# Kernel tuning notes

Hardware: AMD Instinct MI355X
Metric: run time of the kernel (lower is better)

The kernel has to match this reference:

```python
import jax, jax.numpy as jnp
import numpy as np

L, B, C, OUT = 4, 4, 256, 4
H, W = 128, 128
HEADS, DH, G = 8, 32, 64
N = H * W
INNER = HEADS * DH
HID = 4 * C


def _ln(x, w, b, eps=1e-5):
    m = jnp.mean(x, -1, keepdims=True)
    v = jnp.mean((x - m) ** 2, -1, keepdims=True)
    return (x - m) / jnp.sqrt(v + eps) * w + b


def setup_inputs() -> dict:
    key = jax.random.key(0)
    ks = iter(jax.random.split(key, 16))
    nrm = lambda shape, s=0.02: jax.random.normal(next(ks), shape, jnp.float32) * s
    return dict(
        fx=jax.random.normal(next(ks), (B, N, C), jnp.float32),
        ln1_w=jnp.ones((L, C)), ln1_b=jnp.zeros((L, C)),
        convx_w=nrm((L, 3, 3, C, INNER)), convx_b=jnp.zeros((L, INNER)),
        convfx_w=nrm((L, 3, 3, C, INNER)), convfx_b=jnp.zeros((L, INNER)),
        slice_w=nrm((L, DH, G)), slice_b=jnp.zeros((L, G)),
        temperature=0.5 * jnp.ones((L, HEADS)),
        wq=nrm((L, DH, DH)), wk=nrm((L, DH, DH)), wv=nrm((L, DH, DH)),
        wo=nrm((L, INNER, C)), bo=jnp.zeros((L, C)),
        ln2_w=jnp.ones((L, C)), ln2_b=jnp.zeros((L, C)),
        w1=nrm((L, C, HID)), b1=jnp.zeros((L, HID)),
        w2=nrm((L, HID, C)), b2=jnp.zeros((L, C)),
        ln3_w=jnp.ones((C,)), ln3_b=jnp.zeros((C,)),
        w_out=nrm((C, OUT)), b_out=jnp.zeros((OUT,)),
    )


def reference(fx, ln1_w, ln1_b, convx_w, convx_b, convfx_w, convfx_b,
              slice_w, slice_b, temperature, wq, wk, wv, wo, bo,
              ln2_w, ln2_b, w1, b1, w2, b2, ln3_w, ln3_b, w_out, b_out):
    Bb = fx.shape[0]
    scale = DH ** -0.5
    for i in range(L):
        # --- Physics attention (slice attention) ---
        x = _ln(fx, ln1_w[i], ln1_b[i])
        ximg = x.reshape(Bb, H, W, C)  # NHWC
        conv = lambda w, b: jax.lax.conv_general_dilated(
            ximg, w, (1, 1), 'SAME',
            dimension_numbers=('NHWC', 'HWIO', 'NHWC')) + b
        fx_mid = conv(convfx_w[i], convfx_b[i]).reshape(Bb, N, HEADS, DH).transpose(0, 2, 1, 3)  # [B,h,N,d]
        x_mid = conv(convx_w[i], convx_b[i]).reshape(Bb, N, HEADS, DH).transpose(0, 2, 1, 3)
        temp = jnp.clip(temperature[i], 0.1, 5.0)[None, :, None, None]
        logits = (jnp.einsum('bhnd,dg->bhng', x_mid, slice_w[i]) + slice_b[i]) / temp
        sw = jax.nn.softmax(logits, axis=-1)  # [B,h,N,G]
        norm = sw.sum(2)  # [B,h,G]
        st = jnp.einsum('bhnc,bhng->bhgc', fx_mid, sw) / (norm + 1e-5)[..., None]  # [B,h,G,d]
        q = jnp.einsum('bhgc,cd->bhgd', st, wq[i])
        k = jnp.einsum('bhgc,cd->bhgd', st, wk[i])
        v = jnp.einsum('bhgc,cd->bhgd', st, wv[i])
        attn = jax.nn.softmax(jnp.einsum('bhgd,bhkd->bhgk', q, k) * scale, axis=-1)
        ot = jnp.einsum('bhgk,bhkd->bhgd', attn, v)  # [B,h,G,d]
        out_x = jnp.einsum('bhgc,bhng->bhnc', ot, sw)  # deslice back to points
        out_x = out_x.transpose(0, 2, 1, 3).reshape(Bb, N, INNER)
        fx = fx + out_x @ wo[i] + bo[i]
        # --- MLP (n_layers=0, no res inside) ---
        h = _ln(fx, ln2_w[i], ln2_b[i])
        h = jax.nn.gelu(h @ w1[i] + b1[i], approximate=False) @ w2[i] + b2[i]
        fx = fx + h
    # last-layer head
    return _ln(fx, ln3_w, ln3_b) @ w_out + b_out
```

## Files before the change

kernel.cpp:

```cpp
#include <hip/hip_runtime.h>
#include <hip/hip_bf16.h>

typedef __hip_bfloat16 bf16;
typedef __bf16 bfv8 __attribute__((ext_vector_type(8)));
typedef float f32x4 __attribute__((ext_vector_type(4)));

#define BB 4
#define HH 128
#define WWI 128
#define NN 16384
#define CC 256
#define LL 4
#define NHEADS 8
#define DHD 32
#define GG 64
#define INNERC 256
#define HIDD 1024
#define SPLIT 32
#define SSP 16

__device__ __forceinline__ float b2f(bf16 x) { return __bfloat162float(x); }
__device__ __forceinline__ bf16 f2b(float x) { return __float2bfloat16(x); }
__device__ __forceinline__ float us2f(unsigned short v) {
  return __uint_as_float(((unsigned)v) << 16);
}
__device__ __forceinline__ unsigned short b2us(bf16 h) {
  union { bf16 b; unsigned short u; } c; c.b = h; return c.u;
}

__device__ __forceinline__ void async16(void* l, const void* g) {
  __builtin_amdgcn_global_load_lds(
      (const __attribute__((address_space(1))) void*)g,
      (__attribute__((address_space(3))) void*)l, 16, 0, 0);
}

__device__ __forceinline__ float wave_sum(float v) {
#pragma unroll
  for (int off = 32; off > 0; off >>= 1) v += __shfl_down(v, off, 64);
  return v;
}

__device__ __forceinline__ float gelu_exact(float x) {
  return 0.5f * x * (1.0f + erff(x * 0.70710678118654752f));
}

__global__ void transpose_cast_kernel(const float* __restrict__ src, bf16* __restrict__ dst,
                                      int R, int Cm) {
  __shared__ float tile[32][33];
  int tb = blockIdx.z;
  const float* s = src + (size_t)tb * R * Cm;
  bf16* d = dst + (size_t)tb * R * Cm;
  int c0 = blockIdx.x * 32, r0 = blockIdx.y * 32;
  int tx = threadIdx.x & 31, ty = threadIdx.x >> 5;
  for (int rr = ty; rr < 32; rr += 8) {
    int r = r0 + rr, c = c0 + tx;
    tile[rr][tx] = (r < R && c < Cm) ? s[(size_t)r * Cm + c] : 0.f;
  }
  __syncthreads();
  for (int cc = ty; cc < 32; cc += 8) {
    int c = c0 + cc, r = r0 + tx;
    if (c < Cm && r < R) d[(size_t)c * R + r] = f2b(tile[tx][cc]);
  }
}

__global__ __launch_bounds__(256) void ln_kernel(const float* __restrict__ x,
                                                 const float* __restrict__ w,
                                                 const float* __restrict__ b,
                                                 bf16* __restrict__ out) {
  int wid = threadIdx.x >> 6, lane = threadIdx.x & 63;
  int p = blockIdx.x * 4 + wid;
  float4 v = ((const float4*)(x + (size_t)p * CC))[lane];
  float s = v.x + v.y + v.z + v.w;
  float sq = v.x * v.x + v.y * v.y + v.z * v.z + v.w * v.w;
#pragma unroll
  for (int off = 32; off > 0; off >>= 1) {
    s += __shfl_xor(s, off, 64);
    sq += __shfl_xor(sq, off, 64);
  }
  float mean = s * (1.0f / CC);
  float var = sq * (1.0f / CC) - mean * mean;
  float rstd = rsqrtf(var + 1e-5f);
  float4 wv = ((const float4*)w)[lane];
  float4 bv = ((const float4*)b)[lane];
  unsigned short o0 = b2us(f2b((v.x - mean) * rstd * wv.x + bv.x));
  unsigned short o1 = b2us(f2b((v.y - mean) * rstd * wv.y + bv.y));
  unsigned short o2 = b2us(f2b((v.z - mean) * rstd * wv.z + bv.z));
  unsigned short o3 = b2us(f2b((v.w - mean) * rstd * wv.w + bv.w));
  uint2 pk = make_uint2((unsigned)o0 | ((unsigned)o1 << 16),
                        (unsigned)o2 | ((unsigned)o3 << 16));
  ((uint2*)(out + (size_t)p * CC))[lane] = pk;
}

__global__ __launch_bounds__(512, 2) void conv_mfma_kernel(
    const bf16* __restrict__ xln, const bf16* __restrict__ wt,
    const float* __restrict__ bias, bf16* __restrict__ out,
    const float* __restrict__ zbuf) {
  __shared__ __align__(16) unsigned short As[4 * 130 * 64];
  __shared__ __align__(16) unsigned short Bsm[2][256 * 64];
  int bid = blockIdx.x;
  bid = (bid & 7) * 32 + (bid >> 3);
  int h0 = (bid & 63) * 2;
  int b = bid >> 6;
  int t = threadIdx.x, lane = t & 63, wid = t >> 6;
  int r = wid & 1;
  int wn = (wid >> 1) * 64;
  int l15 = lane & 15, l4 = lane >> 4;
  int wu = t & ~63;
  f32x4 acc[8][4];
#pragma unroll
  for (int mi = 0; mi < 8; ++mi)
#pragma unroll
    for (int ni = 0; ni < 4; ++ni) acc[mi][ni] = (f32x4){0.f, 0.f, 0.f, 0.f};
  const bf16* xbase = xln + (size_t)b * NN * CC;

  auto stageB = [&](int buf, int tap, int q) {
#pragma unroll
    for (int k = 0; k < 4; ++k) {
      int u = t + k * 512;
      int n = u >> 3, jp = u & 7, j = jp ^ (n & 7);
      async16(&Bsm[buf][(size_t)(wu + k * 512) * 8],
              wt + ((size_t)(tap * 256 + n)) * 256 + q * 64 + j * 8);
    }
  };

  for (int q = 0; q < 4; ++q) {
#pragma unroll
    for (int k = 0; k < 8; ++k) {
      int u = t + k * 512;
      int jp = u & 7, pc = u >> 3;
      int ar = pc / 130, cl = pc - ar * 130;
      int j = jp ^ (cl & 7);
      int gr = h0 + ar - 1, gc = cl - 1;
      const void* src =
          ((unsigned)gr < 128u && (unsigned)gc < 128u)
              ? (const void*)(xbase + ((size_t)(gr * WWI + gc)) * CC + q * 64 + j * 8)
              : (const void*)zbuf;
      async16(&As[(size_t)(wu + k * 512) * 8], src);
    }
    if (t < 64) {
      int u = t + 4096;
      int jp = u & 7, pc = u >> 3;
      int ar = pc / 130, cl = pc - ar * 130;
      int j = jp ^ (cl & 7);
      int gr = h0 + ar - 1, gc = cl - 1;
      const void* src =
          ((unsigned)gr < 128u && (unsigned)gc < 128u)
              ? (const void*)(xbase + ((size_t)(gr * WWI + gc)) * CC + q * 64 + j * 8)
              : (const void*)zbuf;
      async16(&As[(size_t)4096 * 8], src);
    }
    if (q == 0) stageB(0, 0, 0);
    __syncthreads();

    for (int tap = 0; tap < 9; ++tap) {
      int cur = (q * 9 + tap) & 1;
      if (tap < 8)      stageB(cur ^ 1, tap + 1, q);
      else if (q < 3)   stageB(cur ^ 1, 0, q + 1);
      int ky = tap / 3, kx = tap - ky * 3;
      const unsigned short* Bc = Bsm[cur];
#pragma unroll
      for (int s = 0; s < 2; ++s) {
        bfv8 af[8], bfr[4];
#pragma unroll
        for (int mi = 0; mi < 8; ++mi) {
          int cl = mi * 16 + l15 + kx;
          af[mi] = *(const bfv8*)(&As[((size_t)((ky + r) * 130 + cl)) * 64 +
                                      (((s * 4 + l4) ^ (cl & 7)) << 3)]);
        }
#pragma unroll
        for (int ni = 0; ni < 4; ++ni) {
          int rn = wn + ni * 16 + l15;
          bfr[ni] = *(const bfv8*)(&Bc[(size_t)rn * 64 + (((s * 4 + l4) ^ (rn & 7)) << 3)]);
        }
#pragma unroll
        for (int mi = 0; mi < 8; ++mi)
#pragma unroll
          for (int ni = 0; ni < 4; ++ni)
            acc[mi][ni] = __builtin_amdgcn_mfma_f32_16x16x32_bf16(af[mi], bfr[ni], acc[mi][ni], 0, 0, 0);
      }
      __syncthreads();
    }
  }
  int colB = wn + l15;
  int rowB = l4 * 4;
#pragma unroll
  for (int ni = 0; ni < 4; ++ni) {
    int oc = colB + ni * 16;
    float bv = bias[oc];
#pragma unroll
    for (int mi = 0; mi < 8; ++mi) {
#pragma unroll
      for (int rr = 0; rr < 4; ++rr) {
        int pix = mi * 16 + rowB + rr;
        out[((size_t)(b * NN + (h0 + r) * WWI + pix)) * CC + oc] = f2b(acc[mi][ni][rr] + bv);
      }
    }
  }
}

__global__ __launch_bounds__(512) void gemm_ln_kernel(
    const bf16* __restrict__ A, const bf16* __restrict__ BT,
    const float* __restrict__ bias, float* __restrict__ fx,
    const float* __restrict__ lw, const float* __restrict__ lb,
    bf16* __restrict__ xout) {
  __shared__ __align__(16) unsigned short As[128 * 64];
  __shared__ __align__(16) unsigned short Bs[256 * 64];
  int z = blockIdx.y;
  const bf16* Aa = A + (size_t)z * NN * 512;
  const bf16* Ba = BT + (size_t)z * 256 * 512;
  size_t fb = (size_t)z * NN * 256;
  int m0 = blockIdx.x * 128;
  int t = threadIdx.x, lane = t & 63, wid = t >> 6;
  int wm = (wid & 1) * 64, wn = (wid >> 1) * 64;
  int l15 = lane & 15, q4 = lane >> 4;
  int wu = t & ~63;
  f32x4 acc[4][4];
#pragma unroll
  for (int mi = 0; mi < 4; ++mi)
#pragma unroll
    for (int ni = 0; ni < 4; ++ni) acc[mi][ni] = (f32x4){0.f, 0.f, 0.f, 0.f};

  for (int kb = 0; kb < 512; kb += 64) {
    __syncthreads();
#pragma unroll
    for (int i = 0; i < 2; ++i) {
      int u = t + i * 512;
      int row = u >> 3, jp = u & 7, j = jp ^ (row & 7);
      async16(&As[(size_t)(wu + i * 512) * 8], Aa + (size_t)(m0 + row) * 512 + kb + j * 8);
    }
#pragma unroll
    for (int i = 0; i < 4; ++i) {
      int u = t + i * 512;
      int n = u >> 3, jp = u & 7, j = jp ^ (n & 7);
      async16(&Bs[(size_t)(wu + i * 512) * 8], Ba + (size_t)n * 512 + kb + j * 8);
    }
    __syncthreads();
#pragma unroll
    for (int s = 0; s < 2; ++s) {
      int kgrp = s * 4 + q4;
      bfv8 af[4], bfr[4];
#pragma unroll
      for (int mi = 0; mi < 4; ++mi) {
        int row = wm + mi * 16 + l15;
        af[mi] = *(const bfv8*)(&As[(size_t)row * 64 + ((kgrp ^ (row & 7)) << 3)]);
      }
#pragma unroll
      for (int ni = 0; ni < 4; ++ni) {
        int n = wn + ni * 16 + l15;
        bfr[ni] = *(const bfv8*)(&Bs[(size_t)n * 64 + ((kgrp ^ (n & 7)) << 3)]);
      }
#pragma unroll
      for (int mi = 0; mi < 4; ++mi)
#pragma unroll
        for (int ni = 0; ni < 4; ++ni)
          acc[mi][ni] = __builtin_amdgcn_mfma_f32_16x16x32_bf16(af[mi], bfr[ni], acc[mi][ni], 0, 0, 0);
    }
  }
  __syncthreads();
  float* rs = (float*)As;
  float* rq = rs + 512;
  int cw = wid >> 1;
  int colB = wn + l15;
  float bv[4], lwv[4], lbv[4];
#pragma unroll
  for (int ni = 0; ni < 4; ++ni) {
    bv[ni] = bias[colB + ni * 16];
    lwv[ni] = lw[colB + ni * 16];
    lbv[ni] = lb[colB + ni * 16];
  }
#pragma unroll
  for (int mi = 0; mi < 4; ++mi) {
#pragma unroll
    for (int r = 0; r < 4; ++r) {
      int row = m0 + wm + mi * 16 + q4 * 4 + r;
      float s = 0.f, sq = 0.f;
#pragma unroll
      for (int ni = 0; ni < 4; ++ni) {
        size_t idx = fb + (size_t)row * 256 + colB + ni * 16;
        float v = fx[idx] + acc[mi][ni][r] + bv[ni];
        fx[idx] = v;
        s += v; sq += v * v;
      }
#pragma unroll
      for (int off = 1; off < 16; off <<= 1) {
        s += __shfl_xor(s, off, 64);
        sq += __shfl_xor(sq, off, 64);
      }
      if (l15 == 0) {
        int lrow = wm + mi * 16 + q4 * 4 + r;
        rs[cw * 128 + lrow] = s;
        rq[cw * 128 + lrow] = sq;
      }
    }
  }
  __syncthreads();
#pragma unroll
  for (int mi = 0; mi < 4; ++mi) {
#pragma unroll
    for (int r = 0; r < 4; ++r) {
      int lrow = wm + mi * 16 + q4 * 4 + r;
      float tot = rs[lrow] + rs[128 + lrow] + rs[256 + lrow] + rs[384 + lrow];
      float totq = rq[lrow] + rq[128 + lrow] + rq[256 + lrow] + rq[384 + lrow];
      float mean = tot * (1.0f / CC);
      float var = totq * (1.0f / CC) - mean * mean;
      float rstd = rsqrtf(var + 1e-5f);
      int row = m0 + lrow;
#pragma unroll
      for (int ni = 0; ni < 4; ++ni) {
        size_t idx = fb + (size_t)row * 256 + colB + ni * 16;
        float v = fx[idx];
        xout[idx] = f2b((v - mean) * rstd * lwv[ni] + lbv[ni]);
      }
    }
  }
}

__global__ __launch_bounds__(512, 4) void mlp_fused_kernel(
    const bf16* __restrict__ xln, const bf16* __restrict__ w1t,
    const float* __restrict__ b1, const bf16* __restrict__ w2t,
    const float* __restrict__ b2, float* __restrict__ fx,
    const float* __restrict__ lnw, const float* __restrict__ lnb,
    bf16* __restrict__ xout) {
  __shared__ __align__(16) unsigned short As[64 * 256];
  __shared__ __align__(16) bf16 Hs[64 * 128];
  __shared__ __align__(16) unsigned short Wb[256 * 64];
  int m0 = blockIdx.x * 64;
  int t = threadIdx.x, lane = t & 63, wid = t >> 6;
  int l15 = lane & 15, q4 = lane >> 4;
  int wm2 = (wid & 1) * 32, wn2 = (wid >> 1) * 32;
  int wm = (wid & 1) * 32, wn = (wid >> 1) * 64;

  const unsigned short* xg = (const unsigned short*)xln + (size_t)m0 * 256;
#pragma unroll
  for (int i = 0; i < 4; ++i) {
    int u = t + i * 512;
    int row = u >> 5, v = u & 31;
    int kb = v >> 3, jp = v & 7;
    uint4 val = ((const uint4*)xg)[u];
    ((uint4*)As)[row * 32 + kb * 8 + (jp ^ (row & 7))] = val;
  }

  f32x4 accO[2][4];
#pragma unroll
  for (int mi = 0; mi < 2; ++mi)
#pragma unroll
    for (int ni = 0; ni < 4; ++ni) accO[mi][ni] = (f32x4){0.f, 0.f, 0.f, 0.f};

  for (int j = 0; j < 8; ++j) {
    int hbase = j * 128;
    f32x4 acc2[2][2];
#pragma unroll
    for (int mi = 0; mi < 2; ++mi)
#pragma unroll
      for (int nj = 0; nj < 2; ++nj) acc2[mi][nj] = (f32x4){0.f, 0.f, 0.f, 0.f};
    for (int kb = 0; kb < 4; ++kb) {
      __syncthreads();
#pragma unroll
      for (int i = 0; i < 2; ++i) {
        int u = t + i * 512;
        int n = u >> 3, jp = u & 7;
        uint4 val = *(const uint4*)(w1t + (size_t)(hbase + n) * 256 + kb * 64 + jp * 8);
        ((uint4*)Wb)[n * 8 + (jp ^ (n & 7))] = val;
      }
      __syncthreads();
#pragma unroll
      for (int ks = 0; ks < 2; ++ks) {
        int kgrp = ks * 4 + q4;
        bfv8 af[2], bfr[2];
#pragma unroll
        for (int mi = 0; mi < 2; ++mi) {
          int row = wm2 + mi * 16 + l15;
          af[mi] = *(const bfv8*)(&As[row * 256 + kb * 64 + ((kgrp ^ (row & 7)) << 3)]);
        }
#pragma unroll
        for (int nj = 0; nj < 2; ++nj) {
          int n = wn2 + nj * 16 + l15;
          bfr[nj] = *(const bfv8*)(&Wb[n * 64 + ((kgrp ^ (n & 7)) << 3)]);
        }
#pragma unroll
        for (int mi = 0; mi < 2; ++mi)
#pragma unroll
          for (int nj = 0; nj < 2; ++nj)
            acc2[mi][nj] = __builtin_amdgcn_mfma_f32_16x16x32_bf16(af[mi], bfr[nj], acc2[mi][nj], 0, 0, 0);
      }
    }
#pragma unroll
    for (int nj = 0; nj < 2; ++nj) {
      int coln = wn2 + nj * 16 + l15;
      float bv = b1[hbase + coln];
      int half = coln >> 6, sub = (coln >> 3) & 7, lo = coln & 7;
#pragma unroll
      for (int mi = 0; mi < 2; ++mi) {
#pragma unroll
        for (int r = 0; r < 4; ++r) {
          int row = wm2 + mi * 16 + q4 * 4 + r;
          float v = acc2[mi][nj][r] + bv;
          Hs[row * 128 + half * 64 + (((sub ^ (row & 7)) << 3) + lo)] = f2b(gelu_exact(v));
        }
      }
    }
    for (int kb2 = 0; kb2 < 2; ++kb2) {
      __syncthreads();
#pragma unroll
      for (int i = 0; i < 4; ++i) {
        int u = t + i * 512;
        int n = u >> 3, jp = u & 7;
        uint4 val = *(const uint4*)(w2t + (size_t)n * 1024 + hbase + kb2 * 64 + jp * 8);
        ((uint4*)Wb)[n * 8 + (jp ^ (n & 7))] = val;
      }
      __syncthreads();
#pragma unroll
      for (int ks = 0; ks < 2; ++ks) {
        int kgrp = ks * 4 + q4;
        bfv8 af[2], bfr[4];
#pragma unroll
        for (int mi = 0; mi < 2; ++mi) {
          int row = wm + mi * 16 + l15;
          af[mi] = *(const bfv8*)(&Hs[row * 128 + kb2 * 64 + ((kgrp ^ (row & 7)) << 3)]);
        }
#pragma unroll
        for (int ni = 0; ni < 4; ++ni) {
          int n = wn + ni * 16 + l15;
          bfr[ni] = *(const bfv8*)(&Wb[n * 64 + ((kgrp ^ (n & 7)) << 3)]);
        }
#pragma unroll
        for (int mi = 0; mi < 2; ++mi)
#pragma unroll
          for (int ni = 0; ni < 4; ++ni)
            accO[mi][ni] = __builtin_amdgcn_mfma_f32_16x16x32_bf16(af[mi], bfr[ni], accO[mi][ni], 0, 0, 0);
      }
    }
  }
  float* rs = (float*)As;
  float* rq = rs + 256;
  int cw = wid >> 1;
  int colB = wn + l15;
  float bv[4], lwv[4], lbv[4];
#pragma unroll
  for (int ni = 0; ni < 4; ++ni) {
    bv[ni] = b2[colB + ni * 16];
    if (lnw) { lwv[ni] = lnw[colB + ni * 16]; lbv[ni] = lnb[colB + ni * 16]; }
  }
#pragma unroll
  for (int mi = 0; mi < 2; ++mi) {
#pragma unroll
    for (int r = 0; r < 4; ++r) {
      int row = m0 + wm + mi * 16 + q4 * 4 + r;
      float s = 0.f, sq = 0.f;
#pragma unroll
      for (int ni = 0; ni < 4; ++ni) {
        size_t idx = (size_t)row * 256 + colB + ni * 16;
        float v = fx[idx] + accO[mi][ni][r] + bv[ni];
        fx[idx] = v;
        s += v; sq += v * v;
      }
      if (lnw) {
#pragma unroll
        for (int off = 1; off < 16; off <<= 1) {
          s += __shfl_xor(s, off, 64);
          sq += __shfl_xor(sq, off, 64);
        }
        if (l15 == 0) {
          int lrow = wm + mi * 16 + q4 * 4 + r;
          rs[cw * 64 + lrow] = s;
          rq[cw * 64 + lrow] = sq;
        }
      }
    }
  }
  if (lnw) {
    __syncthreads();
#pragma unroll
    for (int mi = 0; mi < 2; ++mi) {
#pragma unroll
      for (int r = 0; r < 4; ++r) {
        int lrow = wm + mi * 16 + q4 * 4 + r;
        float tot = rs[lrow] + rs[64 + lrow] + rs[128 + lrow] + rs[192 + lrow];
        float totq = rq[lrow] + rq[64 + lrow] + rq[128 + lrow] + rq[192 + lrow];
        float mean = tot * (1.0f / CC);
        float var = totq * (1.0f / CC) - mean * mean;
        float rstd = rsqrtf(var + 1e-5f);
        int row = m0 + lrow;
#pragma unroll
        for (int ni = 0; ni < 4; ++ni) {
          size_t idx = (size_t)row * 256 + colB + ni * 16;
          float v = fx[idx];
          xout[idx] = f2b((v - mean) * rstd * lwv[ni] + lbv[ni]);
        }
      }
    }
  }
}

__global__ __launch_bounds__(256) void slice_softmax_kernel(
    const bf16* __restrict__ xmid, const float* __restrict__ sw_w,
    const float* __restrict__ sw_b, const float* __restrict__ temp,
    bf16* __restrict__ swout) {
  __shared__ float xm[SSP][256];
  int p0 = blockIdx.x * SSP;
  int t = threadIdx.x;
  int g = t & 63, pq = t >> 6;
  float wreg[32];
#pragma unroll
  for (int d = 0; d < 32; ++d) wreg[d] = sw_w[d * 64 + g];
  float bg = sw_b[g];
  float rt[8];
#pragma unroll
  for (int h = 0; h < 8; ++h) rt[h] = 1.0f / fminf(fmaxf(temp[h], 0.1f), 5.0f);
  const unsigned short* xg = (const unsigned short*)xmid + (size_t)p0 * 256;
#pragma unroll
  for (int i2 = t; i2 < SSP * 32; i2 += 256) {
    uint4 v = ((const uint4*)xg)[i2];
    int p = i2 >> 5, c = (i2 & 31) << 3;
    xm[p][c + 0] = us2f((unsigned short)(v.x & 0xffff));
    xm[p][c + 1] = us2f((unsigned short)(v.x >> 16));
    xm[p][c + 2] = us2f((unsigned short)(v.y & 0xffff));
    xm[p][c + 3] = us2f((unsigned short)(v.y >> 16));
    xm[p][c + 4] = us2f((unsigned short)(v.z & 0xffff));
    xm[p][c + 5] = us2f((unsigned short)(v.z >> 16));
    xm[p][c + 6] = us2f((unsigned short)(v.w & 0xffff));
    xm[p][c + 7] = us2f((unsigned short)(v.w >> 16));
  }
  __syncthreads();
  for (int pp2 = 0; pp2 < SSP / 4; ++pp2) {
    int p = pp2 * 4 + pq;
#pragma unroll
    for (int h = 0; h < NHEADS; ++h) {
      float acc = bg;
      const float* xr = &xm[p][h * 32];
#pragma unroll
      for (int d = 0; d < 32; ++d) acc += xr[d] * wreg[d];
      float logit = acc * rt[h];
      float m = logit;
#pragma unroll
      for (int off = 32; off > 0; off >>= 1) m = fmaxf(m, __shfl_xor(m, off, 64));
      float e = __expf(logit - m);
      float s = e;
#pragma unroll
      for (int off = 32; off > 0; off >>= 1) s += __shfl_xor(s, off, 64);
      swout[(size_t)(p0 + p) * 512 + h * 64 + g] = f2b(e / s);
    }
  }
}

__global__ __launch_bounds__(256) void slice_st_kernel(
    const bf16* __restrict__ fxmid, const bf16* __restrict__ sw,
    float* __restrict__ stp, float* __restrict__ normp) {
  __shared__ __align__(16) unsigned short sw_s[64 * 64];
  __shared__ __align__(16) unsigned short fx_s[32 * 64];
  __shared__ float npart[2][64];
  int split = blockIdx.x, h = blockIdx.y, b = blockIdx.z;
  int t = threadIdx.x, w = t >> 6, lane = t & 63;
  int l15 = lane & 15, q4 = lane >> 4;
  int ns0 = split * (NN / SPLIT);
  const int NT = (NN / SPLIT) / 64;
  f32x4 acc0 = {0.f, 0.f, 0.f, 0.f}, acc1 = {0.f, 0.f, 0.f, 0.f};
  float nacc = 0.f;
  const unsigned short* swg = (const unsigned short*)sw + (size_t)b * NN * 512 + h * 64;
  const unsigned short* fxg = (const unsigned short*)fxmid + (size_t)b * NN * 256 + h * 32;

  for (int kt = 0; kt < NT; ++kt) {
    int n0 = ns0 + kt * 64;
    __syncthreads();
    if (w < 2) {
      int g = lane;
#pragma unroll
      for (int i = 0; i < 4; ++i) {
        int j = w + 2 * i;
        const unsigned short* p = swg + (size_t)(n0 + j * 8) * 512 + g;
        unsigned short v0 = p[0],     v1 = p[512],  v2 = p[1024], v3 = p[1536];
        unsigned short v4 = p[2048],  v5 = p[2560], v6 = p[3072], v7 = p[3584];
        nacc += us2f(v0) + us2f(v1) + us2f(v2) + us2f(v3) +
                us2f(v4) + us2f(v5) + us2f(v6) + us2f(v7);
        uint4 pk = make_uint4((unsigned)v0 | ((unsigned)v1 << 16),
                              (unsigned)v2 | ((unsigned)v3 << 16),
                              (unsigned)v4 | ((unsigned)v5 << 16),
                              (unsigned)v6 | ((unsigned)v7 << 16));
        ((uint4*)sw_s)[g * 8 + (j ^ (g & 7))] = pk;
      }
    } else {
      int d = lane & 31, nh = lane >> 5, w3 = w - 2;
#pragma unroll
      for (int i = 0; i < 2; ++i) {
        int nbase = (w3 * 2 + i) * 16 + nh * 8;
        const unsigned short* p = fxg + (size_t)(n0 + nbase) * 256 + d;
        unsigned short v0 = p[0],    v1 = p[256],  v2 = p[512],  v3 = p[768];
        unsigned short v4 = p[1024], v5 = p[1280], v6 = p[1536], v7 = p[1792];
        uint4 pk = make_uint4((unsigned)v0 | ((unsigned)v1 << 16),
                              (unsigned)v2 | ((unsigned)v3 << 16),
                              (unsigned)v4 | ((unsigned)v5 << 16),
                              (unsigned)v6 | ((unsigned)v7 << 16));
        int u = nbase >> 3;
        ((uint4*)fx_s)[d * 8 + (u ^ (d & 7))] = pk;
      }
    }
    __syncthreads();
    int gg = w * 16 + l15;
    int d0 = l15, d1 = 16 + l15;
#pragma unroll
    for (int ks = 0; ks < 2; ++ks) {
      bfv8 af  = ((const bfv8*)sw_s)[gg * 8 + ((ks * 4 + q4) ^ (gg & 7))];
      bfv8 bf0 = ((const bfv8*)fx_s)[d0 * 8 + ((ks * 4 + q4) ^ (d0 & 7))];
      bfv8 bf1 = ((const bfv8*)fx_s)[d1 * 8 + ((ks * 4 + q4) ^ (d1 & 7))];
      acc0 = __builtin_amdgcn_mfma_f32_16x16x32_bf16(af, bf0, acc0, 0, 0, 0);
      acc1 = __builtin_amdgcn_mfma_f32_16x16x32_bf16(af, bf1, acc1, 0, 0, 0);
    }
  }
  if (w < 2) npart[w][lane] = nacc;
  __syncthreads();
  int bh = b * NHEADS + h;
  if (t < 64) normp[(size_t)split * (BB * NHEADS * GG) + bh * 64 + t] = npart[0][t] + npart[1][t];
  size_t base = ((size_t)split * (BB * NHEADS * GG) + bh * 64) * 32;
#pragma unroll
  for (int r = 0; r < 4; ++r) {
    int g = w * 16 + q4 * 4 + r;
    stp[base + (size_t)g * 32 + l15] = acc0[r];
    stp[base + (size_t)g * 32 + 16 + l15] = acc1[r];
  }
}

__global__ __launch_bounds__(256) void attn_wc_kernel(
    const float* __restrict__ stp, const float* __restrict__ normp,
    const float* __restrict__ wq, const float* __restrict__ wk,
    const float* __restrict__ wv, const float* __restrict__ wo,
    bf16* __restrict__ wct) {
  __shared__ float wqs[32 * 32], wks[32 * 32], wvs[32 * 32];
  __shared__ float st[GG][DHD + 1];
  __shared__ float qq[GG][DHD + 1], kk[GG][DHD + 1], vv[GG][DHD + 1];
  __shared__ float pm[GG][GG + 1];
  __shared__ float nrm[GG];
  int bh = blockIdx.x;
  int h2 = bh & 7, bq = bh >> 3;
  int t = threadIdx.x;
  ((float4*)wqs)[t] = ((const float4*)wq)[t];
  ((float4*)wks)[t] = ((const float4*)wk)[t];
  ((float4*)wvs)[t] = ((const float4*)wv)[t];
  float wol[DHD];
#pragma unroll
  for (int d = 0; d < DHD; ++d) wol[d] = wo[(size_t)(h2 * DHD + d) * CC + t];
  if (t < 64) {
    float ns = 0.f;
    for (int s = 0; s < SPLIT; ++s) ns += normp[(size_t)s * (BB * NHEADS * GG) + bh * 64 + t];
    nrm[t] = 1.0f / (ns + 1e-5f);
  }
  __syncthreads();
#pragma unroll
  for (int i = 0; i < 8; ++i) {
    int idx = t + i * 256;
    int g = idx >> 5, d = idx & 31;
    float a = 0.f;
    for (int s = 0; s < SPLIT; ++s)
      a += stp[((size_t)s * (BB * NHEADS * GG) + bh * 64 + g) * 32 + d];
    st[g][d] = a * nrm[g];
  }
  __syncthreads();
#pragma unroll
  for (int i = 0; i < 8; ++i) {
    int idx = t + i * 256;
    int g = idx >> 5, d = idx & 31;
    float aq = 0.f, ak = 0.f, av = 0.f;
#pragma unroll
    for (int c = 0; c < 32; ++c) {
      float sv = st[g][c];
      aq += sv * wqs[c * 32 + d];
      ak += sv * wks[c * 32 + d];
      av += sv * wvs[c * 32 + d];
    }
    qq[g][d] = aq; kk[g][d] = ak; vv[g][d] = av;
  }
  __syncthreads();
  {
    int g = t >> 2, sub = t & 3;
    float sc[16];
    float m = -1e30f;
    const float scale = 0.17677669529663687f;
#pragma unroll
    for (int jj = 0; jj < 16; ++jj) {
      int j = sub * 16 + jj;
      float a = 0.f;
#pragma unroll
      for (int d = 0; d < 32; ++d) a += qq[g][d] * kk[j][d];
      a *= scale;
      sc[jj] = a;
      m = fmaxf(m, a);
    }
    m = fmaxf(m, __shfl_xor(m, 1, 64));
    m = fmaxf(m, __shfl_xor(m, 2, 64));
    float ssum = 0.f;
#pragma unroll
    for (int jj = 0; jj < 16; ++jj) { sc[jj] = __expf(sc[jj] - m); ssum += sc[jj]; }
    ssum += __shfl_xor(ssum, 1, 64);
    ssum += __shfl_xor(ssum, 2, 64);
    float rs = 1.0f / ssum;
#pragma unroll
    for (int jj = 0; jj < 16; ++jj) pm[g][sub * 16 + jj] = sc[jj] * rs;
  }
  __syncthreads();
#pragma unroll
  for (int i = 0; i < 8; ++i) {
    int idx = t + i * 256;
    int g = idx >> 5, d = idx & 31;
    float a = 0.f;
#pragma unroll
    for (int j = 0; j < GG; ++j) a += pm[g][j] * vv[j][d];
    qq[g][d] = a;
  }
  __syncthreads();
  bf16* dst = wct + ((size_t)bq * CC + t) * (NHEADS * GG) + h2 * GG;
#pragma unroll 4
  for (int g = 0; g < GG; ++g) {
    float a = 0.f;
#pragma unroll
    for (int d = 0; d < DHD; ++d) a += wol[d] * qq[g][d];
    dst[g] = f2b(a);
  }
}

__global__ __launch_bounds__(256) void head_kernel(const float* __restrict__ fx,
                                                   const float* __restrict__ w,
                                                   const float* __restrict__ b,
                                                   const float* __restrict__ wout,
                                                   const float* __restrict__ bout,
                                                   float* __restrict__ out) {
  int wid = threadIdx.x >> 6, lane = threadIdx.x & 63;
  int p = blockIdx.x * 4 + wid;
  float4 v = ((const float4*)(fx + (size_t)p * CC))[lane];
  float s = v.x + v.y + v.z + v.w;
  float sq = v.x * v.x + v.y * v.y + v.z * v.z + v.w * v.w;
#pragma unroll
  for (int off = 32; off > 0; off >>= 1) {
    s += __shfl_xor(s, off, 64);
    sq += __shfl_xor(sq, off, 64);
  }
  float mean = s * (1.0f / CC);
  float var = sq * (1.0f / CC) - mean * mean;
  float rstd = rsqrtf(var + 1e-5f);
  float4 wv = ((const float4*)w)[lane];
  float4 bv = ((const float4*)b)[lane];
  float xn0 = (v.x - mean) * rstd * wv.x + bv.x;
  float xn1 = (v.y - mean) * rstd * wv.y + bv.y;
  float xn2 = (v.z - mean) * rstd * wv.z + bv.z;
  float xn3 = (v.w - mean) * rstd * wv.w + bv.w;
  float4 w0 = ((const float4*)wout)[lane * 4 + 0];
  float4 w1 = ((const float4*)wout)[lane * 4 + 1];
  float4 w2 = ((const float4*)wout)[lane * 4 + 2];
  float4 w3 = ((const float4*)wout)[lane * 4 + 3];
  float4 o;
  o.x = xn0 * w0.x + xn1 * w1.x + xn2 * w2.x + xn3 * w3.x;
  o.y = xn0 * w0.y + xn1 * w1.y + xn2 * w2.y + xn3 * w3.y;
  o.z = xn0 * w0.z + xn1 * w1.z + xn2 * w2.z + xn3 * w3.z;
  o.w = xn0 * w0.w + xn1 * w1.w + xn2 * w2.w + xn3 * w3.w;
#pragma unroll
  for (int off = 32; off > 0; off >>= 1) {
    o.x += __shfl_xor(o.x, off, 64);
    o.y += __shfl_xor(o.y, off, 64);
    o.z += __shfl_xor(o.z, off, 64);
    o.w += __shfl_xor(o.w, off, 64);
  }
  if (lane == 0) {
    float4 bo4 = *((const float4*)bout);
    float4 r;
    r.x = o.x + bo4.x; r.y = o.y + bo4.y; r.z = o.z + bo4.z; r.w = o.w + bo4.w;
    ((float4*)out)[p] = r;
  }
}

extern "C" void kernel_launch(void* const* d_in, const int* in_sizes, int n_in,
                              void* d_out, int out_size, void* d_ws, size_t ws_size,
                              hipStream_t stream) {
  const float* fx_in      = (const float*)d_in[0];
  const float* ln1_w      = (const float*)d_in[1];
  const float* ln1_b      = (const float*)d_in[2];
  const float* convx_w    = (const float*)d_in[3];
  const float* convx_b    = (const float*)d_in[4];
  const float* convfx_w   = (const float*)d_in[5];
  const float* convfx_b   = (const float*)d_in[6];
  const float* slice_w    = (const float*)d_in[7];
  const float* slice_b    = (const float*)d_in[8];
  const float* temperature= (const float*)d_in[9];
  const float* wq         = (const float*)d_in[10];
  const float* wk         = (const float*)d_in[11];
  const float* wv         = (const float*)d_in[12];
  const float* wo         = (const float*)d_in[13];
  const float* bo         = (const float*)d_in[14];
  const float* ln2_w      = (const float*)d_in[15];
  const float* ln2_b      = (const float*)d_in[16];
  const float* w1         = (const float*)d_in[17];
  const float* b1         = (const float*)d_in[18];
  const float* w2         = (const float*)d_in[19];
  const float* b2         = (const float*)d_in[20];
  const float* ln3_w      = (const float*)d_in[21];
  const float* ln3_b      = (const float*)d_in[22];
  const float* w_out      = (const float*)d_in[23];
  const float* b_out      = (const float*)d_in[24];
  float* out = (float*)d_out;

  char* ws = (char*)d_ws;
  size_t off = 0;
  auto alloc = [&](size_t bytes) -> void* {
    void* p = ws + off;
    off += (bytes + 255) & ~(size_t)255;
    return p;
  };
  float* fx32  = (float*)alloc((size_t)BB * NN * CC * 4);
  bf16* xln    = (bf16*)alloc((size_t)BB * NN * CC * 2);
  char* uni    = (char*)alloc((size_t)BB * NN * 512 * 2 * 2);
  bf16* xmid   = (bf16*)uni;
  bf16* fxmid  = (bf16*)(uni + (size_t)BB * NN * INNERC * 2);
  bf16* swb    = (bf16*)(uni + (size_t)2 * BB * NN * INNERC * 2);
  float* stp   = (float*)uni;
  float* normp = (float*)(uni + (size_t)SPLIT * BB * NHEADS * GG * DHD * 4);
  bf16* wtx    = (bf16*)alloc((size_t)LL * 9 * CC * INNERC * 2);
  bf16* wtfx   = (bf16*)alloc((size_t)LL * 9 * CC * INNERC * 2);
  bf16* w1t    = (bf16*)alloc((size_t)LL * CC * HIDD * 2);
  bf16* w2t    = (bf16*)alloc((size_t)LL * HIDD * CC * 2);
  bf16* wct    = (bf16*)alloc((size_t)BB * CC * NHEADS * GG * 2);
  float* zbuf  = (float*)alloc(256);
  (void)ws_size; (void)in_sizes; (void)n_in; (void)out_size;

  hipMemsetAsync(zbuf, 0, 256, stream);

  transpose_cast_kernel<<<dim3(8, 8, LL * 9), 256, 0, stream>>>(convx_w, wtx, CC, INNERC);
  transpose_cast_kernel<<<dim3(8, 8, LL * 9), 256, 0, stream>>>(convfx_w, wtfx, CC, INNERC);
  transpose_cast_kernel<<<dim3(32, 8, LL), 256, 0, stream>>>(w1, w1t, CC, HIDD);
  transpose_cast_kernel<<<dim3(8, 32, LL), 256, 0, stream>>>(w2, w2t, HIDD, CC);

  hipMemcpyAsync(fx32, fx_in, (size_t)BB * NN * CC * sizeof(float),
                 hipMemcpyDeviceToDevice, stream);

  const int M = BB * NN;
  ln_kernel<<<M / 4, 256, 0, stream>>>(fx32, ln1_w, ln1_b, xln);
  for (int i = 0; i < LL; ++i) {
    conv_mfma_kernel<<<BB * HH / 2, 512, 0, stream>>>(
        xln, wtfx + (size_t)i * 9 * CC * INNERC, convfx_b + i * INNERC, fxmid,
        (const float*)zbuf);
    conv_mfma_kernel<<<BB * HH / 2, 512, 0, stream>>>(
        xln, wtx + (size_t)i * 9 * CC * INNERC, convx_b + i * INNERC, xmid,
        (const float*)zbuf);
    slice_softmax_kernel<<<M / SSP, 256, 0, stream>>>(
        xmid, slice_w + i * DHD * GG, slice_b + i * GG, temperature + i * NHEADS, swb);
    slice_st_kernel<<<dim3(SPLIT, NHEADS, BB), 256, 0, stream>>>(fxmid, swb, stp, normp);
    attn_wc_kernel<<<BB * NHEADS, 256, 0, stream>>>(
        stp, normp, wq + i * DHD * DHD, wk + i * DHD * DHD, wv + i * DHD * DHD,
        wo + (size_t)i * INNERC * CC, wct);
    gemm_ln_kernel<<<dim3(NN / 128, BB), 512, 0, stream>>>(
        swb, wct, bo + i * CC, fx32, ln2_w + i * CC, ln2_b + i * CC, xln);
    const float* nlw = (i < LL - 1) ? ln1_w + (i + 1) * CC : nullptr;
    const float* nlb = (i < LL - 1) ? ln1_b + (i + 1) * CC : nullptr;
    mlp_fused_kernel<<<M / 64, 512, 0, stream>>>(
        xln, w1t + (size_t)i * CC * HIDD, b1 + i * HIDD,
        w2t + (size_t)i * HIDD * CC, b2 + i * CC, fx32, nlw, nlb, xln);
  }
  head_kernel<<<M / 4, 256, 0, stream>>>(fx32, ln3_w, ln3_b, w_out, b_out, out);
}
```

Measured before the change: 2.394 ms.

## Unfuse next-layer LayerNorm from MLP kernel; keep residual values in registers for LN

The MLP kernel no longer computes the following layer's LayerNorm in its epilogue. It only adds the residual, and a separate ln_kernel launch produces the normalized bf16 input for layers after the first. In gemm_ln_kernel the updated residual values are kept in a register array instead of being re-read from global memory for normalization. This lightens the MLP epilogue (fewer registers, no extra syncthreads) at the cost of an extra kernel launch and an extra full pass over fx. The register array also raises register pressure in gemm_ln.

```diff
diff --git a/kernel.cpp b/kernel.cpp
--- a/kernel.cpp
+++ b/kernel.cpp
@@ -268,6 +268,7 @@
     lwv[ni] = lw[colB + ni * 16];
     lbv[ni] = lb[colB + ni * 16];
   }
+  float vkeep[4][4][4];
 #pragma unroll
   for (int mi = 0; mi < 4; ++mi) {
 #pragma unroll
@@ -279,6 +280,7 @@
         size_t idx = fb + (size_t)row * 256 + colB + ni * 16;
         float v = fx[idx] + acc[mi][ni][r] + bv[ni];
         fx[idx] = v;
+        vkeep[mi][r][ni] = v;
         s += v; sq += v * v;
       }
 #pragma unroll
@@ -308,7 +310,7 @@
 #pragma unroll
       for (int ni = 0; ni < 4; ++ni) {
         size_t idx = fb + (size_t)row * 256 + colB + ni * 16;
-        float v = fx[idx];
+        float v = vkeep[mi][r][ni];
         xout[idx] = f2b((v - mean) * rstd * lwv[ni] + lbv[ni]);
       }
     }
@@ -318,9 +320,7 @@
 __global__ __launch_bounds__(512, 4) void mlp_fused_kernel(
     const bf16* __restrict__ xln, const bf16* __restrict__ w1t,
     const float* __restrict__ b1, const bf16* __restrict__ w2t,
-    const float* __restrict__ b2, float* __restrict__ fx,
-    const float* __restrict__ lnw, const float* __restrict__ lnb,
-    bf16* __restrict__ xout) {
+    const float* __restrict__ b2, float* __restrict__ fx) {
   __shared__ __align__(16) unsigned short As[64 * 256];
   __shared__ __align__(16) bf16 Hs[64 * 128];
   __shared__ __align__(16) unsigned short Wb[256 * 64];
@@ -431,62 +431,16 @@
       }
     }
   }
-  float* rs = (float*)As;
-  float* rq = rs + 256;
-  int cw = wid >> 1;
-  int colB = wn + l15;
-  float bv[4], lwv[4], lbv[4];
 #pragma unroll
   for (int ni = 0; ni < 4; ++ni) {
-    bv[ni] = b2[colB + ni * 16];
-    if (lnw) { lwv[ni] = lnw[colB + ni * 16]; lbv[ni] = lnb[colB + ni * 16]; }
-  }
-#pragma unroll
-  for (int mi = 0; mi < 2; ++mi) {
-#pragma unroll
-    for (int r = 0; r < 4; ++r) {
-      int row = m0 + wm + mi * 16 + q4 * 4 + r;
-      float s = 0.f, sq = 0.f;
-#pragma unroll
-      for (int ni = 0; ni < 4; ++ni) {
-        size_t idx = (size_t)row * 256 + colB + ni * 16;
-        float v = fx[idx] + accO[mi][ni][r] + bv[ni];
-        fx[idx] = v;
-        s += v; sq += v * v;
-      }
-      if (lnw) {
-#pragma unroll
-        for (int off = 1; off < 16; off <<= 1) {
-          s += __shfl_xor(s, off, 64);
-          sq += __shfl_xor(sq, off, 64);
-        }
-        if (l15 == 0) {
-          int lrow = wm + mi * 16 + q4 * 4 + r;
-          rs[cw * 64 + lrow] = s;
-          rq[cw * 64 + lrow] = sq;
-        }
-      }
-    }
-  }
-  if (lnw) {
-    __syncthreads();
+    int col = wn + ni * 16 + l15;
+    float bv = b2[col];
 #pragma unroll
     for (int mi = 0; mi < 2; ++mi) {
 #pragma unroll
       for (int r = 0; r < 4; ++r) {
-        int lrow = wm + mi * 16 + q4 * 4 + r;
-        float tot = rs[lrow] + rs[64 + lrow] + rs[128 + lrow] + rs[192 + lrow];
-        float totq = rq[lrow] + rq[64 + lrow] + rq[128 + lrow] + rq[192 + lrow];
-        float mean = tot * (1.0f / CC);
-        float var = totq * (1.0f / CC) - mean * mean;
-        float rstd = rsqrtf(var + 1e-5f);
-        int row = m0 + lrow;
-#pragma unroll
-        for (int ni = 0; ni < 4; ++ni) {
-          size_t idx = (size_t)row * 256 + colB + ni * 16;
-          float v = fx[idx];
-          xout[idx] = f2b((v - mean) * rstd * lwv[ni] + lbv[ni]);
-        }
+        int row = m0 + wm + mi * 16 + q4 * 4 + r;
+        fx[(size_t)row * 256 + col] += accO[mi][ni][r] + bv;
       }
     }
   }
@@ -845,11 +799,12 @@
         wo + (size_t)i * INNERC * CC, wct);
     gemm_ln_kernel<<<dim3(NN / 128, BB), 512, 0, stream>>>(
         swb, wct, bo + i * CC, fx32, ln2_w + i * CC, ln2_b + i * CC, xln);
-    const float* nlw = (i < LL - 1) ? ln1_w + (i + 1) * CC : nullptr;
-    const float* nlb = (i < LL - 1) ? ln1_b + (i + 1) * CC : nullptr;
     mlp_fused_kernel<<<M / 64, 512, 0, stream>>>(
         xln, w1t + (size_t)i * CC * HIDD, b1 + i * HIDD,
-        w2t + (size_t)i * HIDD * CC, b2 + i * CC, fx32, nlw, nlb, xln);
+        w2t + (size_t)i * HIDD * CC, b2 + i * CC, fx32);
+    if (i < LL - 1)
+      ln_kernel<<<M / 4, 256, 0, stream>>>(fx32, ln1_w + (i + 1) * CC,
+                                           ln1_b + (i + 1) * CC, xln);
   }
   head_kernel<<<M / 4, 256, 0, stream>>>(fx32, ln3_w, ln3_b, w_out, b_out, out);
 }
```

After: 2.252 ms. 5.9% less time.
